# Kernel tuning notes

Measured on AMD Instinct MI355X. Metric: run time of the kernel, lower is better.

The kernel has to match this reference:

```python
import jax, jax.numpy as jnp
import numpy as np

N, E, C, NS, NB, NH = 20000, 320000, 64, 4, 8, 64
AVG_NEIGH = 16.0

def setup_inputs() -> dict:
    key = jax.random.key(0)
    ks = jax.random.split(key, 16)
    inp = {}
    inp['vectors'] = 0.35 * jax.random.normal(ks[0], (E, 3), jnp.float32)
    inp['node_scalars'] = jax.random.normal(ks[1], (N, C), jnp.float32)
    inp['node_vectors'] = jax.random.normal(ks[2], (N, C, 3), jnp.float32)
    inp['node_specie'] = jax.random.randint(ks[3], (N,), 0, NS)
    inp['senders'] = jax.random.randint(ks[4], (E,), 0, N)
    inp['receivers'] = jax.random.randint(ks[5], (E,), 0, N)
    # indexed skip linear: node irreps (64x0e+64x1o) -> 64x0e+64x1o+64x0e (scalars incl. gates)
    inp['W_skip_s'] = jax.random.normal(ks[6], (NS, C, 2 * C), jnp.float32) / np.sqrt(C)
    inp['W_skip_v'] = jax.random.normal(ks[7], (NS, C, C), jnp.float32) / np.sqrt(C)
    inp['W_up_s'] = jax.random.normal(ks[8], (C, C), jnp.float32) / np.sqrt(C)
    inp['W_up_v'] = jax.random.normal(ks[9], (C, C), jnp.float32) / np.sqrt(C)
    inp['W_mlp0'] = jax.random.normal(ks[10], (NB, NH), jnp.float32) / np.sqrt(NB)
    inp['W_mlp1'] = jax.random.normal(ks[11], (NH, NH), jnp.float32) / np.sqrt(NH)
    inp['W_mlp2'] = jax.random.normal(ks[12], (NH, 4 * C), jnp.float32) / np.sqrt(NH)
    inp['W_down_s'] = jax.random.normal(ks[13], (2 * C, 2 * C), jnp.float32) / np.sqrt(2 * C)
    inp['W_down_v'] = jax.random.normal(ks[14], (2 * C, C), jnp.float32) / np.sqrt(2 * C)
    return inp


def _forward(vectors, node_scalars, node_vectors, node_specie, senders, receivers,
             W_skip_s, W_skip_v, W_up_s, W_up_v, W_mlp0, W_mlp1, W_mlp2, W_down_s, W_down_v):
    n = node_scalars.shape[0]
    # --- self connection (specie-indexed linear) ---
    skip_s = jnp.einsum('ni,nio->no', node_scalars, W_skip_s[node_specie])   # [N,128]
    skip_v = jnp.einsum('nim,nio->nom', node_vectors, W_skip_v[node_specie]) # [N,64,3]
    # --- linear up ---
    s = node_scalars @ W_up_s                                  # [N,64]
    v = jnp.einsum('nim,io->nom', node_vectors, W_up_v)        # [N,64,3]
    ms, mv = s[senders], v[senders]                            # gather -> [E,64], [E,64,3]
    # --- spherical harmonics l=1, component normalization (|Y|=sqrt(3)) ---
    lengths = jnp.linalg.norm(vectors, axis=1, keepdims=True)  # [E,1]
    vhat = vectors / jnp.where(lengths == 0.0, 1.0, lengths)
    Y = jnp.sqrt(3.0) * vhat                                   # [E,3]
    # --- tensor product, filter_ir_out = {0e,1o} ---
    t1 = ms[:, :, None] * Y[:, None, :]                        # 0e x 1o -> 1o [E,64,3]
    t0 = jnp.einsum('ecm,em->ec', mv, Y) / jnp.sqrt(3.0)       # 1o x 1o -> 0e [E,64]
    msg_s = jnp.concatenate([ms, t0], axis=1)                  # [E,128]
    msg_v = jnp.concatenate([mv, t1], axis=1)                  # [E,128,3]
    # --- radial basis * polynomial envelope -> MLP ---
    x = lengths[:, 0]
    nvec = jnp.arange(1, NB + 1, dtype=vectors.dtype)
    safe_x = jnp.where(x == 0.0, 1.0, x)
    bess = jnp.sqrt(2.0) * jnp.sin(nvec * jnp.pi * x[:, None]) / safe_x[:, None]  # [E,8]
    u = jnp.clip(x, 0.0, 1.0)
    env = jnp.where(x < 1.0, 1.0 - 28.0 * u**6 + 48.0 * u**7 - 21.0 * u**8, 0.0)  # poly_envelope(5,2)
    h = jax.nn.swish((bess * env[:, None]) @ W_mlp0)
    h = jax.nn.swish(h @ W_mlp1)
    mix = h @ W_mlp2                                           # [E,256] = 128x0e + 128x1o weights
    mix = jnp.where(lengths == 0.0, 0.0, mix)
    msg_s = msg_s * mix[:, : 2 * C]
    msg_v = msg_v * mix[:, 2 * C :, None]
    # --- scatter-add to receivers, normalize by sqrt(avg_num_neighbors) ---
    inv = 1.0 / jnp.sqrt(AVG_NEIGH)
    agg_s = jnp.zeros((n, 2 * C), msg_s.dtype).at[receivers].add(msg_s) * inv
    agg_v = jnp.zeros((n, 2 * C, 3), msg_v.dtype).at[receivers].add(msg_v) * inv
    # --- linear down to 64x0e + 64x1o + 64x0e(gates) ---
    out_s = agg_s @ W_down_s + skip_s                          # [N,128]
    out_v = jnp.einsum('nim,io->nom', agg_v, W_down_v) + skip_v  # [N,64,3]
    # --- gate: swish on scalars, swish(gates) modulates vectors ---
    scal = jax.nn.swish(out_s[:, :C])
    gates = jax.nn.swish(out_s[:, C:])
    vec = out_v * gates[:, :, None]
    return jnp.concatenate([scal, vec.reshape(n, 3 * C)], axis=1)  # [N,256]


def reference(vectors, node_scalars, node_vectors, node_specie, senders, receivers,
              W_skip_s, W_skip_v, W_up_s, W_up_v, W_mlp0, W_mlp1, W_mlp2, W_down_s, W_down_v):
    return _forward(vectors, node_scalars, node_vectors, node_specie, senders, receivers,
                    W_skip_s, W_skip_v, W_up_s, W_up_v, W_mlp0, W_mlp1, W_mlp2, W_down_s, W_down_v)
```

## Files before the change

kernel.cpp:

```cpp
#include <hip/hip_runtime.h>
#include <math.h>

#define PI_F        3.14159265358979323846f
#define SQRT2_F     1.41421356237309515f
#define SQRT3_F     1.73205080756887729f
#define INV_SQRT3_F 0.57735026918962576f
#define INV_AVG     0.25f

#define N_NODES 20000
#define N_EDGES 320000

typedef float v2f __attribute__((ext_vector_type(2)));
typedef float v4f __attribute__((ext_vector_type(4)));

__device__ __forceinline__ float swish_f(float x) {
    return x / (1.f + __expf(-x));
}

__global__ __launch_bounds__(256, 8) void k_zero_cnt(int* __restrict__ cnt) {
    const int i = blockIdx.x * 256 + threadIdx.x;
    if (i < N_NODES) cnt[i] = 0;
}
__global__ __launch_bounds__(256, 8) void k_hist(const int* __restrict__ rcv,
                                                 int* __restrict__ cnt) {
    const int e = blockIdx.x * 256 + threadIdx.x;
    if (e < N_EDGES) atomicAdd(&cnt[rcv[e]], 1);
}
__global__ __launch_bounds__(1024) void k_scan(const int* __restrict__ cnt,
                                               int* __restrict__ cursor) {
    __shared__ int part[1024];
    const int t = threadIdx.x;
    const int base = t * 20;
    int s = 0;
    #pragma unroll
    for (int j = 0; j < 20; ++j) {
        const int idx = base + j;
        if (idx < N_NODES) s += cnt[idx];
    }
    part[t] = s;
    __syncthreads();
    for (int d = 1; d < 1024; d <<= 1) {
        const int v = (t >= d) ? part[t - d] : 0;
        __syncthreads();
        part[t] += v;
        __syncthreads();
    }
    int run = (t == 0) ? 0 : part[t - 1];
    for (int j = 0; j < 20; ++j) {
        const int idx = base + j;
        if (idx < N_NODES) { cursor[idx] = run; run += cnt[idx]; }
    }
}
__global__ __launch_bounds__(256, 8) void k_scatter(const int* __restrict__ rcv,
                                                    int* __restrict__ cursor,
                                                    int* __restrict__ perm) {
    const int e = blockIdx.x * 256 + threadIdx.x;
    if (e < N_EDGES) {
        const int pos = atomicAdd(&cursor[rcv[e]], 1);
        perm[pos] = e;
    }
}

__global__ __launch_bounds__(256) void k_node_up(
    const float* __restrict__ ns, const float* __restrict__ nv,
    const float* __restrict__ Wus, const float* __restrict__ Wuv,
    float* __restrict__ s_up, float* __restrict__ v_up,
    float* __restrict__ agg_s, float* __restrict__ agg_v)
{
    __shared__ v4f actu[16*64];

    const int tid  = threadIdx.x;
    const int lane = tid & 63;
    const int wq   = __builtin_amdgcn_readfirstlane(tid >> 6);
    const int nb   = blockIdx.x * 16;

    #pragma unroll
    for (int k = 0; k < 4; ++k) {
        const int idx = k*256 + tid;
        const int n = idx >> 6, i = idx & 63;
        const float* nvp = nv + (nb + n)*192 + 3*i;
        actu[idx] = (v4f){ns[(nb + n)*64 + i], nvp[0], nvp[1], nvp[2]};
    }
    __syncthreads();

    float acc[4] = {0.f, 0.f, 0.f, 0.f};
    float a0[4] = {}, a1[4] = {}, a2[4] = {};
    const v4f* aw = actu + wq*4*64;
    for (int i = 0; i < 64; ++i) {
        const float wu = Wus[i*64 + lane];
        const float wv = Wuv[i*64 + lane];
        #pragma unroll
        for (int j = 0; j < 4; ++j) {
            const v4f a = aw[j*64 + i];
            acc[j] = fmaf(a.x, wu, acc[j]);
            a0[j]  = fmaf(a.y, wv, a0[j]);
            a1[j]  = fmaf(a.z, wv, a1[j]);
            a2[j]  = fmaf(a.w, wv, a2[j]);
        }
    }
    const int cc = lane & 15, nt = lane >> 4;
    #pragma unroll
    for (int j = 0; j < 4; ++j) {
        const int n = nb + wq*4 + j;
        s_up[n*64 + cc*4 + nt] = acc[j];
        float* vq = v_up + n*192 + cc*12 + nt*3;
        vq[0] = a0[j]; vq[1] = a1[j]; vq[2] = a2[j];
        agg_s[n*128 + lane]      = 0.f;
        agg_s[n*128 + 64 + lane] = 0.f;
        #pragma unroll
        for (int k = 0; k < 6; ++k) agg_v[n*384 + k*64 + lane] = 0.f;
    }
}

__global__ __launch_bounds__(256, 4) void k_edge(
    const float* __restrict__ vecs,
    const int*   __restrict__ snd_idx, const int* __restrict__ rcv_idx,
    const int*   __restrict__ perm,
    const float* __restrict__ W0, const float* __restrict__ W1,
    const float* __restrict__ W2,
    const float* __restrict__ s_up, const float* __restrict__ v_up,
    float* __restrict__ agg_s, float* __restrict__ agg_v)
{
    __shared__ float hv[64*68];

    const int tid  = threadIdx.x;
    const int lane = tid & 63;
    const int wq   = __builtin_amdgcn_readfirstlane(tid >> 6);
    const int e0   = blockIdx.x * 64;
    const int c    = lane & 15, q = lane >> 4;

    const int pe_l  = perm[e0 + lane];
    const int rcv_l = rcv_idx[pe_l];
    const int snd_l = snd_idx[pe_l];
    const float vx_l = vecs[pe_l*3+0], vy_l = vecs[pe_l*3+1], vz_l = vecs[pe_l*3+2];
    const float x_l  = sqrtf(vx_l*vx_l + vy_l*vy_l + vz_l*vz_l);
    const float sx_l = (x_l == 0.f) ? 1.f : x_l;
    const float ys_l = SQRT3_F / sx_l;
    const float Y0_l = vx_l * ys_l, Y1_l = vy_l * ys_l, Y2_l = vz_l * ys_l;

    float s1_l, c1_l;
    __sincosf(PI_F * x_l, &s1_l, &c1_l);
    float pref_l;
    {
        const float u  = fminf(x_l, 1.f);
        const float u2 = u*u, u3 = u2*u;
        const float u6 = u3*u3, u7 = u6*u, u8 = u6*u2;
        const float env = (x_l < 1.f) ? (1.f - 28.f*u6 + 48.f*u7 - 21.f*u8) : 0.f;
        pref_l = (x_l == 0.f) ? 0.f : (SQRT2_F * env / sx_l);
    }

    float h1o[16];
    #pragma unroll 4
    for (int t = 0; t < 16; ++t) {
        const int le = wq*16 + t;
        const float sn0  = __shfl(s1_l, le);
        const float twoc = 2.f * __shfl(c1_l, le);
        const float pref = __shfl(pref_l, le);
        float acc1 = 0.f;
        float sn = sn0, snm1 = 0.f;
        #pragma unroll
        for (int b = 0; b < 8; ++b) {
            acc1 = fmaf(sn, W0[b*64 + lane], acc1);
            const float snext = fmaf(twoc, sn, -snm1);
            snm1 = sn; sn = snext;
        }
        h1o[t] = swish_f(pref * acc1);
    }
    {
        float* dst = hv + lane*68 + wq*16;
        #pragma unroll
        for (int k = 0; k < 4; ++k)
            ((v4f*)dst)[k] = (v4f){h1o[4*k], h1o[4*k+1], h1o[4*k+2], h1o[4*k+3]};
    }

    {
        v2f acc2[8];
        #pragma unroll
        for (int tp = 0; tp < 8; ++tp) acc2[tp] = (v2f){0.f, 0.f};
        const float* hbase = hv + wq*16;
        for (int i = 0; i < 64; ++i) {
            const float w = W1[i*64 + lane];
            const v2f wv = {w, w};
            const v4f* hp4 = (const v4f*)(hbase + i*68);
            #pragma unroll
            for (int k = 0; k < 4; ++k) {
                const v4f h4 = hp4[k];
                const v2f hlo = __builtin_shufflevector(h4, h4, 0, 1);
                const v2f hhi = __builtin_shufflevector(h4, h4, 2, 3);
                acc2[2*k]   = __builtin_elementwise_fma(hlo, wv, acc2[2*k]);
                acc2[2*k+1] = __builtin_elementwise_fma(hhi, wv, acc2[2*k+1]);
            }
        }
        float* dst = hv + lane*68 + wq*16;
        #pragma unroll
        for (int k = 0; k < 4; ++k)
            ((v4f*)dst)[k] = (v4f){swish_f(acc2[2*k][0]),   swish_f(acc2[2*k][1]),
                                   swish_f(acc2[2*k+1][0]), swish_f(acc2[2*k+1][1])};
    }
    __syncthreads();

    v2f mixp[8][4];
    #pragma unroll
    for (int tp = 0; tp < 8; ++tp)
        #pragma unroll
        for (int j = 0; j < 4; ++j) mixp[tp][j] = (v2f){0.f, 0.f};
    {
        const float* W2c = W2 + 64*wq + c;
        const float* hq  = hv + q*16;
        for (int i = 0; i < 64; ++i) {
            const float w0 = W2c[i*256 +  0];
            const float w1 = W2c[i*256 + 16];
            const float w2 = W2c[i*256 + 32];
            const float w3 = W2c[i*256 + 48];
            const v2f w0v = {w0,w0}, w1v = {w1,w1}, w2v = {w2,w2}, w3v = {w3,w3};
            const v4f* hp4 = (const v4f*)(hq + i*68);
            #pragma unroll
            for (int k = 0; k < 4; ++k) {
                const v4f h4 = hp4[k];
                const v2f hlo = __builtin_shufflevector(h4, h4, 0, 1);
                const v2f hhi = __builtin_shufflevector(h4, h4, 2, 3);
                mixp[2*k][0]   = __builtin_elementwise_fma(hlo, w0v, mixp[2*k][0]);
                mixp[2*k][1]   = __builtin_elementwise_fma(hlo, w1v, mixp[2*k][1]);
                mixp[2*k][2]   = __builtin_elementwise_fma(hlo, w2v, mixp[2*k][2]);
                mixp[2*k][3]   = __builtin_elementwise_fma(hlo, w3v, mixp[2*k][3]);
                mixp[2*k+1][0] = __builtin_elementwise_fma(hhi, w0v, mixp[2*k+1][0]);
                mixp[2*k+1][1] = __builtin_elementwise_fma(hhi, w1v, mixp[2*k+1][1]);
                mixp[2*k+1][2] = __builtin_elementwise_fma(hhi, w2v, mixp[2*k+1][2]);
                mixp[2*k+1][3] = __builtin_elementwise_fma(hhi, w3v, mixp[2*k+1][3]);
            }
        }
    }
    #define MIXR(t,j) (mixp[(t)>>1][j][(t)&1])

    int cur = -1;
    if (wq == 0) {
        float ra0=0.f, ra1=0.f, ra2=0.f, ra3=0.f;
        #pragma unroll
        for (int t = 0; t < 16; ++t) {
            const int sl  = (lane & 48) + t;
            const int rcv = __shfl(rcv_l, sl);
            const int snd = __shfl(snd_l, sl);
            if (rcv != cur) {
                if (cur >= 0) {
                    float* p = agg_s + cur*128 + c;
                    unsafeAtomicAdd(p,      ra0);
                    unsafeAtomicAdd(p + 16, ra1);
                    unsafeAtomicAdd(p + 32, ra2);
                    unsafeAtomicAdd(p + 48, ra3);
                }
                ra0 = ra1 = ra2 = ra3 = 0.f; cur = rcv;
            }
            const v4f sv = *(const v4f*)(s_up + snd*64 + c*4);
            ra0 = fmaf(sv.x, MIXR(t,0), ra0);
            ra1 = fmaf(sv.y, MIXR(t,1), ra1);
            ra2 = fmaf(sv.z, MIXR(t,2), ra2);
            ra3 = fmaf(sv.w, MIXR(t,3), ra3);
        }
        float* p = agg_s + cur*128 + c;
        unsafeAtomicAdd(p,      ra0);
        unsafeAtomicAdd(p + 16, ra1);
        unsafeAtomicAdd(p + 32, ra2);
        unsafeAtomicAdd(p + 48, ra3);
    } else if (wq == 1) {
        float ra0=0.f, ra1=0.f, ra2=0.f, ra3=0.f;
        #pragma unroll
        for (int t = 0; t < 16; ++t) {
            const int sl  = (lane & 48) + t;
            const int rcv = __shfl(rcv_l, sl);
            const int snd = __shfl(snd_l, sl);
            const float Y0 = __shfl(Y0_l, sl), Y1 = __shfl(Y1_l, sl), Y2 = __shfl(Y2_l, sl);
            if (rcv != cur) {
                if (cur >= 0) {
                    float* p = agg_s + cur*128 + 64 + c;
                    unsafeAtomicAdd(p,      ra0);
                    unsafeAtomicAdd(p + 16, ra1);
                    unsafeAtomicAdd(p + 32, ra2);
                    unsafeAtomicAdd(p + 48, ra3);
                }
                ra0 = ra1 = ra2 = ra3 = 0.f; cur = rcv;
            }
            const float* vb = v_up + snd*192 + c*12;
            const v4f f0 = *(const v4f*)(vb);
            const v4f f1 = *(const v4f*)(vb + 4);
            const v4f f2 = *(const v4f*)(vb + 8);
            const float t00 = (f0.x*Y0 + f0.y*Y1 + f0.z*Y2) * INV_SQRT3_F;
            const float t01 = (f0.w*Y0 + f1.x*Y1 + f1.y*Y2) * INV_SQRT3_F;
            const float t02 = (f1.z*Y0 + f1.w*Y1 + f2.x*Y2) * INV_SQRT3_F;
            const float t03 = (f2.y*Y0 + f2.z*Y1 + f2.w*Y2) * INV_SQRT3_F;
            ra0 = fmaf(t00, MIXR(t,0), ra0);
            ra1 = fmaf(t01, MIXR(t,1), ra1);
            ra2 = fmaf(t02, MIXR(t,2), ra2);
            ra3 = fmaf(t03, MIXR(t,3), ra3);
        }
        float* p = agg_s + cur*128 + 64 + c;
        unsafeAtomicAdd(p,      ra0);
        unsafeAtomicAdd(p + 16, ra1);
        unsafeAtomicAdd(p + 32, ra2);
        unsafeAtomicAdd(p + 48, ra3);
    } else if (wq == 2) {
        float rv[4][3];
        #pragma unroll
        for (int i = 0; i < 4; ++i) { rv[i][0]=0.f; rv[i][1]=0.f; rv[i][2]=0.f; }
        #pragma unroll
        for (int t = 0; t < 16; ++t) {
            const int sl  = (lane & 48) + t;
            const int rcv = __shfl(rcv_l, sl);
            const int snd = __shfl(snd_l, sl);
            if (rcv != cur) {
                if (cur >= 0) {
                    float* p = agg_v + cur*384 + c*3;
                    #pragma unroll
                    for (int ntl = 0; ntl < 4; ++ntl)
                        #pragma unroll
                        for (int m = 0; m < 3; ++m)
                            unsafeAtomicAdd(p + ntl*48 + m, rv[ntl][m]);
                }
                #pragma unroll
                for (int i = 0; i < 4; ++i) { rv[i][0]=0.f; rv[i][1]=0.f; rv[i][2]=0.f; }
                cur = rcv;
            }
            const float* vb = v_up + snd*192 + c*12;
            const v4f f0 = *(const v4f*)(vb);
            const v4f f1 = *(const v4f*)(vb + 4);
            const v4f f2 = *(const v4f*)(vb + 8);
            const float mx0 = MIXR(t,0);
            const float mx1 = MIXR(t,1);
            const float mx2 = MIXR(t,2);
            const float mx3 = MIXR(t,3);
            rv[0][0] = fmaf(f0.x, mx0, rv[0][0]);
            rv[0][1] = fmaf(f0.y, mx0, rv[0][1]);
            rv[0][2] = fmaf(f0.z, mx0, rv[0][2]);
            rv[1][0] = fmaf(f0.w, mx1, rv[1][0]);
            rv[1][1] = fmaf(f1.x, mx1, rv[1][1]);
            rv[1][2] = fmaf(f1.y, mx1, rv[1][2]);
            rv[2][0] = fmaf(f1.z, mx2, rv[2][0]);
            rv[2][1] = fmaf(f1.w, mx2, rv[2][1]);
            rv[2][2] = fmaf(f2.x, mx2, rv[2][2]);
            rv[3][0] = fmaf(f2.y, mx3, rv[3][0]);
            rv[3][1] = fmaf(f2.z, mx3, rv[3][1]);
            rv[3][2] = fmaf(f2.w, mx3, rv[3][2]);
        }
        float* p = agg_v + cur*384 + c*3;
        #pragma unroll
        for (int ntl = 0; ntl < 4; ++ntl)
            #pragma unroll
            for (int m = 0; m < 3; ++m)
                unsafeAtomicAdd(p + ntl*48 + m, rv[ntl][m]);
    } else {
        float rv[4][3];
        #pragma unroll
        for (int i = 0; i < 4; ++i) { rv[i][0]=0.f; rv[i][1]=0.f; rv[i][2]=0.f; }
        #pragma unroll
        for (int t = 0; t < 16; ++t) {
            const int sl  = (lane & 48) + t;
            const int rcv = __shfl(rcv_l, sl);
            const int snd = __shfl(snd_l, sl);
            const float Y0 = __shfl(Y0_l, sl), Y1 = __shfl(Y1_l, sl), Y2 = __shfl(Y2_l, sl);
            if (rcv != cur) {
                if (cur >= 0) {
                    float* p = agg_v + cur*384 + 192 + c*3;
                    #pragma unroll
                    for (int ntl = 0; ntl < 4; ++ntl)
                        #pragma unroll
                        for (int m = 0; m < 3; ++m)
                            unsafeAtomicAdd(p + ntl*48 + m, rv[ntl][m]);
                }
                #pragma unroll
                for (int i = 0; i < 4; ++i) { rv[i][0]=0.f; rv[i][1]=0.f; rv[i][2]=0.f; }
                cur = rcv;
            }
            const v4f sv = *(const v4f*)(s_up + snd*64 + c*4);
            const float mm0 = sv.x * MIXR(t,0);
            const float mm1 = sv.y * MIXR(t,1);
            const float mm2 = sv.z * MIXR(t,2);
            const float mm3 = sv.w * MIXR(t,3);
            rv[0][0] = fmaf(mm0, Y0, rv[0][0]);
            rv[0][1] = fmaf(mm0, Y1, rv[0][1]);
            rv[0][2] = fmaf(mm0, Y2, rv[0][2]);
            rv[1][0] = fmaf(mm1, Y0, rv[1][0]);
            rv[1][1] = fmaf(mm1, Y1, rv[1][1]);
            rv[1][2] = fmaf(mm1, Y2, rv[1][2]);
            rv[2][0] = fmaf(mm2, Y0, rv[2][0]);
            rv[2][1] = fmaf(mm2, Y1, rv[2][1]);
            rv[2][2] = fmaf(mm2, Y2, rv[2][2]);
            rv[3][0] = fmaf(mm3, Y0, rv[3][0]);
            rv[3][1] = fmaf(mm3, Y1, rv[3][1]);
            rv[3][2] = fmaf(mm3, Y2, rv[3][2]);
        }
        float* p = agg_v + cur*384 + 192 + c*3;
        #pragma unroll
        for (int ntl = 0; ntl < 4; ++ntl)
            #pragma unroll
            for (int m = 0; m < 3; ++m)
                unsafeAtomicAdd(p + ntl*48 + m, rv[ntl][m]);
    }
    #undef MIXR
}

__global__ __launch_bounds__(256) void k_node_down(
    const float* __restrict__ ns, const float* __restrict__ nv,
    const int*   __restrict__ spec_idx,
    const float* __restrict__ Wds, const float* __restrict__ Wdv,
    const float* __restrict__ Wsks, const float* __restrict__ Wskv,
    const float* __restrict__ agg_s, const float* __restrict__ agg_v,
    float* __restrict__ out)
{
    __shared__ v4f act[16*128];
    __shared__ v4f skp[16*64];
    __shared__ int bord[16];

    const int tid  = threadIdx.x;
    const int lane = tid & 63;
    const int wq   = __builtin_amdgcn_readfirstlane(tid >> 6);
    const int nb   = blockIdx.x * 16;

    if (tid < 16) {
        const int sp = spec_idx[nb + tid];
        int rank = 0;
        for (int j = 0; j < 16; ++j) {
            const int spj = spec_idx[nb + j];
            if (spj < sp || (spj == sp && j < tid)) ++rank;
        }
        bord[rank] = tid;
    }

    #pragma unroll
    for (int k = 0; k < 8; ++k) {
        const int idx = k*256 + tid;
        const int n = idx >> 7, i = idx & 127;
        const float a = agg_s[(nb + n)*128 + i] * INV_AVG;
        const float* av = agg_v + (nb + n)*384 + 3*i;
        act[idx] = (v4f){a, av[0]*INV_AVG, av[1]*INV_AVG, av[2]*INV_AVG};
    }
    #pragma unroll
    for (int k = 0; k < 4; ++k) {
        const int idx = k*256 + tid;
        const int n = idx >> 6, i = idx & 63;
        const float* nvp = nv + (nb + n)*192 + 3*i;
        skp[idx] = (v4f){ns[(nb + n)*64 + i], nvp[0], nvp[1], nvp[2]};
    }
    __syncthreads();

    int ln[4];
    #pragma unroll
    for (int j = 0; j < 4; ++j)
        ln[j] = bord[wq*4 + j];

    float s0[4] = {}, s1[4] = {}, v0[4] = {}, v1[4] = {}, v2[4] = {};

    for (int i = 0; i < 128; ++i) {
        const float wd0 = Wds[i*128 + lane];
        const float wd1 = Wds[i*128 + 64 + lane];
        const float wdv = Wdv[i*64 + lane];
        #pragma unroll
        for (int j = 0; j < 4; ++j) {
            const v4f a = act[ln[j]*128 + i];
            s0[j] = fmaf(a.x, wd0, s0[j]);
            s1[j] = fmaf(a.x, wd1, s1[j]);
            v0[j] = fmaf(a.y, wdv, v0[j]);
            v1[j] = fmaf(a.z, wdv, v1[j]);
            v2[j] = fmaf(a.w, wdv, v2[j]);
        }
    }

    const float* Ws_j[4]; const float* Wv_j[4];
    #pragma unroll
    for (int j = 0; j < 4; ++j) {
        const int spec = __builtin_amdgcn_readfirstlane(spec_idx[nb + ln[j]]);
        Ws_j[j] = Wsks + spec*8192;
        Wv_j[j] = Wskv + spec*4096;
    }
    for (int i = 0; i < 64; ++i) {
        #pragma unroll
        for (int j = 0; j < 4; ++j) {
            const v4f a = skp[ln[j]*64 + i];
            s0[j] = fmaf(a.x, Ws_j[j][i*128 + lane], s0[j]);
            s1[j] = fmaf(a.x, Ws_j[j][i*128 + 64 + lane], s1[j]);
            const float wv = Wv_j[j][i*64 + lane];
            v0[j] = fmaf(a.y, wv, v0[j]);
            v1[j] = fmaf(a.z, wv, v1[j]);
            v2[j] = fmaf(a.w, wv, v2[j]);
        }
    }

    #pragma unroll
    for (int j = 0; j < 4; ++j) {
        const int n = nb + ln[j];
        const float scal = swish_f(s0[j]);
        const float gate = swish_f(s1[j]);
        out[n*256 + lane]            = scal;
        out[n*256 + 64 + lane*3 + 0] = v0[j] * gate;
        out[n*256 + 64 + lane*3 + 1] = v1[j] * gate;
        out[n*256 + 64 + lane*3 + 2] = v2[j] * gate;
    }
}

extern "C" void kernel_launch(void* const* d_in, const int* in_sizes, int n_in,
                              void* d_out, int out_size, void* d_ws, size_t ws_size,
                              hipStream_t stream)
{
    (void)in_sizes; (void)n_in; (void)out_size; (void)ws_size;

    const float* vectors      = (const float*)d_in[0];
    const float* node_scalars = (const float*)d_in[1];
    const float* node_vectors = (const float*)d_in[2];
    const int*   node_specie  = (const int*)d_in[3];
    const int*   senders      = (const int*)d_in[4];
    const int*   receivers    = (const int*)d_in[5];
    const float* W_skip_s     = (const float*)d_in[6];
    const float* W_skip_v     = (const float*)d_in[7];
    const float* W_up_s       = (const float*)d_in[8];
    const float* W_up_v       = (const float*)d_in[9];
    const float* W_mlp0       = (const float*)d_in[10];
    const float* W_mlp1       = (const float*)d_in[11];
    const float* W_mlp2       = (const float*)d_in[12];
    const float* W_down_s     = (const float*)d_in[13];
    const float* W_down_v     = (const float*)d_in[14];
    float* out = (float*)d_out;

    float* ws    = (float*)d_ws;
    float* s_up  = ws;
    float* v_up  = s_up + 1280000;
    float* agg_s = v_up + 3840000;
    float* agg_v = agg_s + 2560000;
    int*   perm  = (int*)(agg_v + 7680000);
    int*   cnt    = (int*)agg_s;
    int*   cursor = cnt + 20000;

    hipLaunchKernelGGL(k_zero_cnt, dim3(79),   dim3(256),  0, stream, cnt);
    hipLaunchKernelGGL(k_hist,     dim3(1250), dim3(256),  0, stream, receivers, cnt);
    hipLaunchKernelGGL(k_scan,     dim3(1),    dim3(1024), 0, stream, cnt, cursor);
    hipLaunchKernelGGL(k_scatter,  dim3(1250), dim3(256),  0, stream, receivers, cursor, perm);

    hipLaunchKernelGGL(k_node_up, dim3(1250), dim3(256), 0, stream,
        node_scalars, node_vectors, W_up_s, W_up_v, s_up, v_up, agg_s, agg_v);
    hipLaunchKernelGGL(k_edge, dim3(5000), dim3(256), 0, stream,
        vectors, senders, receivers, perm, W_mlp0, W_mlp1, W_mlp2,
        s_up, v_up, agg_s, agg_v);
    hipLaunchKernelGGL(k_node_down, dim3(1250), dim3(256), 0, stream,
        node_scalars, node_vectors, node_specie, W_down_s, W_down_v,
        W_skip_s, W_skip_v, agg_s, agg_v, out);
}
```

Baseline: 485.8 us.

## Cut k_edge register pressure via LDS edge metadata and half-split mix accumulation

Per-edge metadata (receiver, sender, Y, sin/cos, prefactor) is written to shared memory instead of being held in registers and broadcast with shuffles. The W2 mix matmul and scatter now run in two halves of 8 edges, which halves the mix accumulator array. Launch bounds rise from 4 to 6 waves so register use must fit a higher occupancy target. This reloads W2 twice and may emit extra atomics at the half boundary. Separately, k_node_down drops its per-block species sort and processes nodes in natural order, which removes that setup work but may make the skip-weight loads less uniform within a wave.

```diff
diff --git a/kernel.cpp b/kernel.cpp
--- a/kernel.cpp
+++ b/kernel.cpp
@@ -112,7 +112,7 @@
     }
 }
 
-__global__ __launch_bounds__(256, 4) void k_edge(
+__global__ __launch_bounds__(256, 6) void k_edge(
     const float* __restrict__ vecs,
     const int*   __restrict__ snd_idx, const int* __restrict__ rcv_idx,
     const int*   __restrict__ perm,
@@ -122,42 +122,44 @@
     float* __restrict__ agg_s, float* __restrict__ agg_v)
 {
     __shared__ float hv[64*68];
+    __shared__ v4f   meta[64*2];
 
     const int tid  = threadIdx.x;
     const int lane = tid & 63;
     const int wq   = __builtin_amdgcn_readfirstlane(tid >> 6);
     const int e0   = blockIdx.x * 64;
     const int c    = lane & 15, q = lane >> 4;
-
-    const int pe_l  = perm[e0 + lane];
-    const int rcv_l = rcv_idx[pe_l];
-    const int snd_l = snd_idx[pe_l];
-    const float vx_l = vecs[pe_l*3+0], vy_l = vecs[pe_l*3+1], vz_l = vecs[pe_l*3+2];
-    const float x_l  = sqrtf(vx_l*vx_l + vy_l*vy_l + vz_l*vz_l);
-    const float sx_l = (x_l == 0.f) ? 1.f : x_l;
-    const float ys_l = SQRT3_F / sx_l;
-    const float Y0_l = vx_l * ys_l, Y1_l = vy_l * ys_l, Y2_l = vz_l * ys_l;
-
-    float s1_l, c1_l;
-    __sincosf(PI_F * x_l, &s1_l, &c1_l);
-    float pref_l;
+    const float* mb = (const float*)meta;
+
     {
-        const float u  = fminf(x_l, 1.f);
+        const int pe  = perm[e0 + lane];
+        const int rcv = rcv_idx[pe];
+        const int snd = snd_idx[pe];
+        const float vx = vecs[pe*3+0], vy = vecs[pe*3+1], vz = vecs[pe*3+2];
+        const float x  = sqrtf(vx*vx + vy*vy + vz*vz);
+        const float sx = (x == 0.f) ? 1.f : x;
+        const float ys = SQRT3_F / sx;
+        float s1, c1;
+        __sincosf(PI_F * x, &s1, &c1);
+        const float u  = fminf(x, 1.f);
         const float u2 = u*u, u3 = u2*u;
         const float u6 = u3*u3, u7 = u6*u, u8 = u6*u2;
-        const float env = (x_l < 1.f) ? (1.f - 28.f*u6 + 48.f*u7 - 21.f*u8) : 0.f;
-        pref_l = (x_l == 0.f) ? 0.f : (SQRT2_F * env / sx_l);
+        const float env = (x < 1.f) ? (1.f - 28.f*u6 + 48.f*u7 - 21.f*u8) : 0.f;
+        const float pref = (x == 0.f) ? 0.f : (SQRT2_F * env / sx);
+        meta[lane*2 + 0] = (v4f){__int_as_float(rcv), __int_as_float(snd),
+                                 vx*ys, vy*ys};
+        meta[lane*2 + 1] = (v4f){vz*ys, s1, c1, pref};
     }
 
     float h1o[16];
     #pragma unroll 4
     for (int t = 0; t < 16; ++t) {
         const int le = wq*16 + t;
-        const float sn0  = __shfl(s1_l, le);
-        const float twoc = 2.f * __shfl(c1_l, le);
-        const float pref = __shfl(pref_l, le);
+        const v4f m1 = meta[le*2 + 1];
+        const float pref = m1.w;
+        const float twoc = 2.f * m1.z;
         float acc1 = 0.f;
-        float sn = sn0, snm1 = 0.f;
+        float sn = m1.y, snm1 = 0.f;
         #pragma unroll
         for (int b = 0; b < 8; ++b) {
             acc1 = fmaf(sn, W0[b*64 + lane], acc1);
@@ -199,202 +201,211 @@
     }
     __syncthreads();
 
-    v2f mixp[8][4];
-    #pragma unroll
-    for (int tp = 0; tp < 8; ++tp)
-        #pragma unroll
-        for (int j = 0; j < 4; ++j) mixp[tp][j] = (v2f){0.f, 0.f};
-    {
-        const float* W2c = W2 + 64*wq + c;
-        const float* hq  = hv + q*16;
-        for (int i = 0; i < 64; ++i) {
-            const float w0 = W2c[i*256 +  0];
-            const float w1 = W2c[i*256 + 16];
-            const float w2 = W2c[i*256 + 32];
-            const float w3 = W2c[i*256 + 48];
-            const v2f w0v = {w0,w0}, w1v = {w1,w1}, w2v = {w2,w2}, w3v = {w3,w3};
-            const v4f* hp4 = (const v4f*)(hq + i*68);
-            #pragma unroll
-            for (int k = 0; k < 4; ++k) {
-                const v4f h4 = hp4[k];
-                const v2f hlo = __builtin_shufflevector(h4, h4, 0, 1);
-                const v2f hhi = __builtin_shufflevector(h4, h4, 2, 3);
-                mixp[2*k][0]   = __builtin_elementwise_fma(hlo, w0v, mixp[2*k][0]);
-                mixp[2*k][1]   = __builtin_elementwise_fma(hlo, w1v, mixp[2*k][1]);
-                mixp[2*k][2]   = __builtin_elementwise_fma(hlo, w2v, mixp[2*k][2]);
-                mixp[2*k][3]   = __builtin_elementwise_fma(hlo, w3v, mixp[2*k][3]);
-                mixp[2*k+1][0] = __builtin_elementwise_fma(hhi, w0v, mixp[2*k+1][0]);
-                mixp[2*k+1][1] = __builtin_elementwise_fma(hhi, w1v, mixp[2*k+1][1]);
-                mixp[2*k+1][2] = __builtin_elementwise_fma(hhi, w2v, mixp[2*k+1][2]);
-                mixp[2*k+1][3] = __builtin_elementwise_fma(hhi, w3v, mixp[2*k+1][3]);
+    #pragma unroll
+    for (int hf = 0; hf < 2; ++hf) {
+        v2f mixp[4][4];
+        #pragma unroll
+        for (int tp = 0; tp < 4; ++tp)
+            #pragma unroll
+            for (int j = 0; j < 4; ++j) mixp[tp][j] = (v2f){0.f, 0.f};
+        {
+            const float* W2c = W2 + 64*wq + c;
+            const float* hq  = hv + q*16 + hf*8;
+            for (int i = 0; i < 64; ++i) {
+                const float w0 = W2c[i*256 +  0];
+                const float w1 = W2c[i*256 + 16];
+                const float w2 = W2c[i*256 + 32];
+                const float w3 = W2c[i*256 + 48];
+                const v2f w0v = {w0,w0}, w1v = {w1,w1}, w2v = {w2,w2}, w3v = {w3,w3};
+                const v4f* hp4 = (const v4f*)(hq + i*68);
+                #pragma unroll
+                for (int k = 0; k < 2; ++k) {
+                    const v4f h4 = hp4[k];
+                    const v2f hlo = __builtin_shufflevector(h4, h4, 0, 1);
+                    const v2f hhi = __builtin_shufflevector(h4, h4, 2, 3);
+                    mixp[2*k][0]   = __builtin_elementwise_fma(hlo, w0v, mixp[2*k][0]);
+                    mixp[2*k][1]   = __builtin_elementwise_fma(hlo, w1v, mixp[2*k][1]);
+                    mixp[2*k][2]   = __builtin_elementwise_fma(hlo, w2v, mixp[2*k][2]);
+                    mixp[2*k][3]   = __builtin_elementwise_fma(hlo, w3v, mixp[2*k][3]);
+                    mixp[2*k+1][0] = __builtin_elementwise_fma(hhi, w0v, mixp[2*k+1][0]);
+                    mixp[2*k+1][1] = __builtin_elementwise_fma(hhi, w1v, mixp[2*k+1][1]);
+                    mixp[2*k+1][2] = __builtin_elementwise_fma(hhi, w2v, mixp[2*k+1][2]);
+                    mixp[2*k+1][3] = __builtin_elementwise_fma(hhi, w3v, mixp[2*k+1][3]);
+                }
             }
         }
-    }
-    #define MIXR(t,j) (mixp[(t)>>1][j][(t)&1])
-
-    int cur = -1;
-    if (wq == 0) {
-        float ra0=0.f, ra1=0.f, ra2=0.f, ra3=0.f;
-        #pragma unroll
-        for (int t = 0; t < 16; ++t) {
-            const int sl  = (lane & 48) + t;
-            const int rcv = __shfl(rcv_l, sl);
-            const int snd = __shfl(snd_l, sl);
-            if (rcv != cur) {
-                if (cur >= 0) {
-                    float* p = agg_s + cur*128 + c;
-                    unsafeAtomicAdd(p,      ra0);
-                    unsafeAtomicAdd(p + 16, ra1);
-                    unsafeAtomicAdd(p + 32, ra2);
-                    unsafeAtomicAdd(p + 48, ra3);
+        #define MIXR(t,j) (mixp[(t)>>1][j][(t)&1])
+
+        int cur = -1;
+        if (wq == 0) {
+            float ra0=0.f, ra1=0.f, ra2=0.f, ra3=0.f;
+            #pragma unroll
+            for (int t = 0; t < 8; ++t) {
+                const int el = (lane & 48) + hf*8 + t;
+                const v2f rs = *(const v2f*)(mb + el*8);
+                const int rcv = __float_as_int(rs.x);
+                const int snd = __float_as_int(rs.y);
+                if (rcv != cur) {
+                    if (cur >= 0) {
+                        float* p = agg_s + cur*128 + c;
+                        unsafeAtomicAdd(p,      ra0);
+                        unsafeAtomicAdd(p + 16, ra1);
+                        unsafeAtomicAdd(p + 32, ra2);
+                        unsafeAtomicAdd(p + 48, ra3);
+                    }
+                    ra0 = ra1 = ra2 = ra3 = 0.f; cur = rcv;
                 }
-                ra0 = ra1 = ra2 = ra3 = 0.f; cur = rcv;
+                const v4f sv = *(const v4f*)(s_up + snd*64 + c*4);
+                ra0 = fmaf(sv.x, MIXR(t,0), ra0);
+                ra1 = fmaf(sv.y, MIXR(t,1), ra1);
+                ra2 = fmaf(sv.z, MIXR(t,2), ra2);
+                ra3 = fmaf(sv.w, MIXR(t,3), ra3);
             }
-            const v4f sv = *(const v4f*)(s_up + snd*64 + c*4);
-            ra0 = fmaf(sv.x, MIXR(t,0), ra0);
-            ra1 = fmaf(sv.y, MIXR(t,1), ra1);
-            ra2 = fmaf(sv.z, MIXR(t,2), ra2);
-            ra3 = fmaf(sv.w, MIXR(t,3), ra3);
-        }
-        float* p = agg_s + cur*128 + c;
-        unsafeAtomicAdd(p,      ra0);
-        unsafeAtomicAdd(p + 16, ra1);
-        unsafeAtomicAdd(p + 32, ra2);
-        unsafeAtomicAdd(p + 48, ra3);
-    } else if (wq == 1) {
-        float ra0=0.f, ra1=0.f, ra2=0.f, ra3=0.f;
-        #pragma unroll
-        for (int t = 0; t < 16; ++t) {
-            const int sl  = (lane & 48) + t;
-            const int rcv = __shfl(rcv_l, sl);
-            const int snd = __shfl(snd_l, sl);
-            const float Y0 = __shfl(Y0_l, sl), Y1 = __shfl(Y1_l, sl), Y2 = __shfl(Y2_l, sl);
-            if (rcv != cur) {
-                if (cur >= 0) {
-                    float* p = agg_s + cur*128 + 64 + c;
-                    unsafeAtomicAdd(p,      ra0);
-                    unsafeAtomicAdd(p + 16, ra1);
-                    unsafeAtomicAdd(p + 32, ra2);
-                    unsafeAtomicAdd(p + 48, ra3);
+            float* p = agg_s + cur*128 + c;
+            unsafeAtomicAdd(p,      ra0);
+            unsafeAtomicAdd(p + 16, ra1);
+            unsafeAtomicAdd(p + 32, ra2);
+            unsafeAtomicAdd(p + 48, ra3);
+        } else if (wq == 1) {
+            float ra0=0.f, ra1=0.f, ra2=0.f, ra3=0.f;
+            #pragma unroll
+            for (int t = 0; t < 8; ++t) {
+                const int el = (lane & 48) + hf*8 + t;
+                const v4f m0 = meta[el*2];
+                const float Y2 = mb[el*8 + 4];
+                const int rcv = __float_as_int(m0.x);
+                const int snd = __float_as_int(m0.y);
+                const float Y0 = m0.z, Y1 = m0.w;
+                if (rcv != cur) {
+                    if (cur >= 0) {
+                        float* p = agg_s + cur*128 + 64 + c;
+                        unsafeAtomicAdd(p,      ra0);
+                        unsafeAtomicAdd(p + 16, ra1);
+                        unsafeAtomicAdd(p + 32, ra2);
+                        unsafeAtomicAdd(p + 48, ra3);
+                    }
+                    ra0 = ra1 = ra2 = ra3 = 0.f; cur = rcv;
                 }
-                ra0 = ra1 = ra2 = ra3 = 0.f; cur = rcv;
+                const float* vb = v_up + snd*192 + c*12;
+                const v4f f0 = *(const v4f*)(vb);
+                const v4f f1 = *(const v4f*)(vb + 4);
+                const v4f f2 = *(const v4f*)(vb + 8);
+                const float t00 = (f0.x*Y0 + f0.y*Y1 + f0.z*Y2) * INV_SQRT3_F;
+                const float t01 = (f0.w*Y0 + f1.x*Y1 + f1.y*Y2) * INV_SQRT3_F;
+                const float t02 = (f1.z*Y0 + f1.w*Y1 + f2.x*Y2) * INV_SQRT3_F;
+                const float t03 = (f2.y*Y0 + f2.z*Y1 + f2.w*Y2) * INV_SQRT3_F;
+                ra0 = fmaf(t00, MIXR(t,0), ra0);
+                ra1 = fmaf(t01, MIXR(t,1), ra1);
+                ra2 = fmaf(t02, MIXR(t,2), ra2);
+                ra3 = fmaf(t03, MIXR(t,3), ra3);
             }
-            const float* vb = v_up + snd*192 + c*12;
-            const v4f f0 = *(const v4f*)(vb);
-            const v4f f1 = *(const v4f*)(vb + 4);
-            const v4f f2 = *(const v4f*)(vb + 8);
-            const float t00 = (f0.x*Y0 + f0.y*Y1 + f0.z*Y2) * INV_SQRT3_F;
-            const float t01 = (f0.w*Y0 + f1.x*Y1 + f1.y*Y2) * INV_SQRT3_F;
-            const float t02 = (f1.z*Y0 + f1.w*Y1 + f2.x*Y2) * INV_SQRT3_F;
-            const float t03 = (f2.y*Y0 + f2.z*Y1 + f2.w*Y2) * INV_SQRT3_F;
-            ra0 = fmaf(t00, MIXR(t,0), ra0);
-            ra1 = fmaf(t01, MIXR(t,1), ra1);
-            ra2 = fmaf(t02, MIXR(t,2), ra2);
-            ra3 = fmaf(t03, MIXR(t,3), ra3);
-        }
-        float* p = agg_s + cur*128 + 64 + c;
-        unsafeAtomicAdd(p,      ra0);
-        unsafeAtomicAdd(p + 16, ra1);
-        unsafeAtomicAdd(p + 32, ra2);
-        unsafeAtomicAdd(p + 48, ra3);
-    } else if (wq == 2) {
-        float rv[4][3];
-        #pragma unroll
-        for (int i = 0; i < 4; ++i) { rv[i][0]=0.f; rv[i][1]=0.f; rv[i][2]=0.f; }
-        #pragma unroll
-        for (int t = 0; t < 16; ++t) {
-            const int sl  = (lane & 48) + t;
-            const int rcv = __shfl(rcv_l, sl);
-            const int snd = __shfl(snd_l, sl);
-            if (rcv != cur) {
-                if (cur >= 0) {
-                    float* p = agg_v + cur*384 + c*3;
+            float* p = agg_s + cur*128 + 64 + c;
+            unsafeAtomicAdd(p,      ra0);
+            unsafeAtomicAdd(p + 16, ra1);
+            unsafeAtomicAdd(p + 32, ra2);
+            unsafeAtomicAdd(p + 48, ra3);
+        } else if (wq == 2) {
+            float rv[4][3];
+            #pragma unroll
+            for (int i = 0; i < 4; ++i) { rv[i][0]=0.f; rv[i][1]=0.f; rv[i][2]=0.f; }
+            #pragma unroll
+            for (int t = 0; t < 8; ++t) {
+                const int el = (lane & 48) + hf*8 + t;
+                const v2f rs = *(const v2f*)(mb + el*8);
+                const int rcv = __float_as_int(rs.x);
+                const int snd = __float_as_int(rs.y);
+                if (rcv != cur) {
+                    if (cur >= 0) {
+                        float* p = agg_v + cur*384 + c*3;
+                        #pragma unroll
+                        for (int ntl = 0; ntl < 4; ++ntl)
+                            #pragma unroll
+                            for (int m = 0; m < 3; ++m)
+                                unsafeAtomicAdd(p + ntl*48 + m, rv[ntl][m]);
+                    }
                     #pragma unroll
-                    for (int ntl = 0; ntl < 4; ++ntl)
+                    for (int i = 0; i < 4; ++i) { rv[i][0]=0.f; rv[i][1]=0.f; rv[i][2]=0.f; }
+                    cur = rcv;
+                }
+                const float* vb = v_up + snd*192 + c*12;
+                const v4f f0 = *(const v4f*)(vb);
+                const v4f f1 = *(const v4f*)(vb + 4);
+                const v4f f2 = *(const v4f*)(vb + 8);
+                const float mx0 = MIXR(t,0);
+                const float mx1 = MIXR(t,1);
+                const float mx2 = MIXR(t,2);
+                const float mx3 = MIXR(t,3);
+                rv[0][0] = fmaf(f0.x, mx0, rv[0][0]);
+                rv[0][1] = fmaf(f0.y, mx0, rv[0][1]);
+                rv[0][2] = fmaf(f0.z, mx0, rv[0][2]);
+                rv[1][0] = fmaf(f0.w, mx1, rv[1][0]);
+                rv[1][1] = fmaf(f1.x, mx1, rv[1][1]);
+                rv[1][2] = fmaf(f1.y, mx1, rv[1][2]);
+                rv[2][0] = fmaf(f1.z, mx2, rv[2][0]);
+                rv[2][1] = fmaf(f1.w, mx2, rv[2][1]);
+                rv[2][2] = fmaf(f2.x, mx2, rv[2][2]);
+                rv[3][0] = fmaf(f2.y, mx3, rv[3][0]);
+                rv[3][1] = fmaf(f2.z, mx3, rv[3][1]);
+                rv[3][2] = fmaf(f2.w, mx3, rv[3][2]);
+            }
+            float* p = agg_v + cur*384 + c*3;
+            #pragma unroll
+            for (int ntl = 0; ntl < 4; ++ntl)
+                #pragma unroll
+                for (int m = 0; m < 3; ++m)
+                    unsafeAtomicAdd(p + ntl*48 + m, rv[ntl][m]);
+        } else {
+            float rv[4][3];
+            #pragma unroll
+            for (int i = 0; i < 4; ++i) { rv[i][0]=0.f; rv[i][1]=0.f; rv[i][2]=0.f; }
+            #pragma unroll
+            for (int t = 0; t < 8; ++t) {
+                const int el = (lane & 48) + hf*8 + t;
+                const v4f m0 = meta[el*2];
+                const float Y2 = mb[el*8 + 4];
+                const int rcv = __float_as_int(m0.x);
+                const int snd = __float_as_int(m0.y);
+                const float Y0 = m0.z, Y1 = m0.w;
+                if (rcv != cur) {
+                    if (cur >= 0) {
+                        float* p = agg_v + cur*384 + 192 + c*3;
                         #pragma unroll
-                        for (int m = 0; m < 3; ++m)
-                            unsafeAtomicAdd(p + ntl*48 + m, rv[ntl][m]);
+                        for (int ntl = 0; ntl < 4; ++ntl)
+                            #pragma unroll
+                            for (int m = 0; m < 3; ++m)
+                                unsafeAtomicAdd(p + ntl*48 + m, rv[ntl][m]);
+                    }
+                    #pragma unroll
+                    for (int i = 0; i < 4; ++i) { rv[i][0]=0.f; rv[i][1]=0.f; rv[i][2]=0.f; }
+                    cur = rcv;
                 }
+                const v4f sv = *(const v4f*)(s_up + snd*64 + c*4);
+                const float mm0 = sv.x * MIXR(t,0);
+                const float mm1 = sv.y * MIXR(t,1);
+                const float mm2 = sv.z * MIXR(t,2);
+                const float mm3 = sv.w * MIXR(t,3);
+                rv[0][0] = fmaf(mm0, Y0, rv[0][0]);
+                rv[0][1] = fmaf(mm0, Y1, rv[0][1]);
+                rv[0][2] = fmaf(mm0, Y2, rv[0][2]);
+                rv[1][0] = fmaf(mm1, Y0, rv[1][0]);
+                rv[1][1] = fmaf(mm1, Y1, rv[1][1]);
+                rv[1][2] = fmaf(mm1, Y2, rv[1][2]);
+                rv[2][0] = fmaf(mm2, Y0, rv[2][0]);
+                rv[2][1] = fmaf(mm2, Y1, rv[2][1]);
+                rv[2][2] = fmaf(mm2, Y2, rv[2][2]);
+                rv[3][0] = fmaf(mm3, Y0, rv[3][0]);
+                rv[3][1] = fmaf(mm3, Y1, rv[3][1]);
+                rv[3][2] = fmaf(mm3, Y2, rv[3][2]);
+            }
+            float* p = agg_v + cur*384 + 192 + c*3;
+            #pragma unroll
+            for (int ntl = 0; ntl < 4; ++ntl)
                 #pragma unroll
-                for (int i = 0; i < 4; ++i) { rv[i][0]=0.f; rv[i][1]=0.f; rv[i][2]=0.f; }
-                cur = rcv;
-            }
-            const float* vb = v_up + snd*192 + c*12;
-            const v4f f0 = *(const v4f*)(vb);
-            const v4f f1 = *(const v4f*)(vb + 4);
-            const v4f f2 = *(const v4f*)(vb + 8);
-            const float mx0 = MIXR(t,0);
-            const float mx1 = MIXR(t,1);
-            const float mx2 = MIXR(t,2);
-            const float mx3 = MIXR(t,3);
-            rv[0][0] = fmaf(f0.x, mx0, rv[0][0]);
-            rv[0][1] = fmaf(f0.y, mx0, rv[0][1]);
-            rv[0][2] = fmaf(f0.z, mx0, rv[0][2]);
-            rv[1][0] = fmaf(f0.w, mx1, rv[1][0]);
-            rv[1][1] = fmaf(f1.x, mx1, rv[1][1]);
-            rv[1][2] = fmaf(f1.y, mx1, rv[1][2]);
-            rv[2][0] = fmaf(f1.z, mx2, rv[2][0]);
-            rv[2][1] = fmaf(f1.w, mx2, rv[2][1]);
-            rv[2][2] = fmaf(f2.x, mx2, rv[2][2]);
-            rv[3][0] = fmaf(f2.y, mx3, rv[3][0]);
-            rv[3][1] = fmaf(f2.z, mx3, rv[3][1]);
-            rv[3][2] = fmaf(f2.w, mx3, rv[3][2]);
-        }
-        float* p = agg_v + cur*384 + c*3;
-        #pragma unroll
-        for (int ntl = 0; ntl < 4; ++ntl)
-            #pragma unroll
-            for (int m = 0; m < 3; ++m)
-                unsafeAtomicAdd(p + ntl*48 + m, rv[ntl][m]);
-    } else {
-        float rv[4][3];
-        #pragma unroll
-        for (int i = 0; i < 4; ++i) { rv[i][0]=0.f; rv[i][1]=0.f; rv[i][2]=0.f; }
-        #pragma unroll
-        for (int t = 0; t < 16; ++t) {
-            const int sl  = (lane & 48) + t;
-            const int rcv = __shfl(rcv_l, sl);
-            const int snd = __shfl(snd_l, sl);
-            const float Y0 = __shfl(Y0_l, sl), Y1 = __shfl(Y1_l, sl), Y2 = __shfl(Y2_l, sl);
-            if (rcv != cur) {
-                if (cur >= 0) {
-                    float* p = agg_v + cur*384 + 192 + c*3;
-                    #pragma unroll
-                    for (int ntl = 0; ntl < 4; ++ntl)
-                        #pragma unroll
-                        for (int m = 0; m < 3; ++m)
-                            unsafeAtomicAdd(p + ntl*48 + m, rv[ntl][m]);
-                }
-                #pragma unroll
-                for (int i = 0; i < 4; ++i) { rv[i][0]=0.f; rv[i][1]=0.f; rv[i][2]=0.f; }
-                cur = rcv;
-            }
-            const v4f sv = *(const v4f*)(s_up + snd*64 + c*4);
-            const float mm0 = sv.x * MIXR(t,0);
-            const float mm1 = sv.y * MIXR(t,1);
-            const float mm2 = sv.z * MIXR(t,2);
-            const float mm3 = sv.w * MIXR(t,3);
-            rv[0][0] = fmaf(mm0, Y0, rv[0][0]);
-            rv[0][1] = fmaf(mm0, Y1, rv[0][1]);
-            rv[0][2] = fmaf(mm0, Y2, rv[0][2]);
-            rv[1][0] = fmaf(mm1, Y0, rv[1][0]);
-            rv[1][1] = fmaf(mm1, Y1, rv[1][1]);
-            rv[1][2] = fmaf(mm1, Y2, rv[1][2]);
-            rv[2][0] = fmaf(mm2, Y0, rv[2][0]);
-            rv[2][1] = fmaf(mm2, Y1, rv[2][1]);
-            rv[2][2] = fmaf(mm2, Y2, rv[2][2]);
-            rv[3][0] = fmaf(mm3, Y0, rv[3][0]);
-            rv[3][1] = fmaf(mm3, Y1, rv[3][1]);
-            rv[3][2] = fmaf(mm3, Y2, rv[3][2]);
-        }
-        float* p = agg_v + cur*384 + 192 + c*3;
-        #pragma unroll
-        for (int ntl = 0; ntl < 4; ++ntl)
-            #pragma unroll
-            for (int m = 0; m < 3; ++m)
-                unsafeAtomicAdd(p + ntl*48 + m, rv[ntl][m]);
-    }
-    #undef MIXR
+                for (int m = 0; m < 3; ++m)
+                    unsafeAtomicAdd(p + ntl*48 + m, rv[ntl][m]);
+        }
+        #undef MIXR
+    }
 }
 
 __global__ __launch_bounds__(256) void k_node_down(
@@ -407,22 +418,11 @@
 {
     __shared__ v4f act[16*128];
     __shared__ v4f skp[16*64];
-    __shared__ int bord[16];
 
     const int tid  = threadIdx.x;
     const int lane = tid & 63;
     const int wq   = __builtin_amdgcn_readfirstlane(tid >> 6);
     const int nb   = blockIdx.x * 16;
-
-    if (tid < 16) {
-        const int sp = spec_idx[nb + tid];
-        int rank = 0;
-        for (int j = 0; j < 16; ++j) {
-            const int spj = spec_idx[nb + j];
-            if (spj < sp || (spj == sp && j < tid)) ++rank;
-        }
-        bord[rank] = tid;
-    }
 
     #pragma unroll
     for (int k = 0; k < 8; ++k) {
@@ -441,20 +441,16 @@
     }
     __syncthreads();
 
-    int ln[4];
-    #pragma unroll
-    for (int j = 0; j < 4; ++j)
-        ln[j] = bord[wq*4 + j];
-
     float s0[4] = {}, s1[4] = {}, v0[4] = {}, v1[4] = {}, v2[4] = {};
 
+    const v4f* aw = act + wq*4*128;
     for (int i = 0; i < 128; ++i) {
         const float wd0 = Wds[i*128 + lane];
         const float wd1 = Wds[i*128 + 64 + lane];
         const float wdv = Wdv[i*64 + lane];
         #pragma unroll
         for (int j = 0; j < 4; ++j) {
-            const v4f a = act[ln[j]*128 + i];
+            const v4f a = aw[j*128 + i];
             s0[j] = fmaf(a.x, wd0, s0[j]);
             s1[j] = fmaf(a.x, wd1, s1[j]);
             v0[j] = fmaf(a.y, wdv, v0[j]);
@@ -463,17 +459,19 @@
         }
     }
 
+    const int n0 = nb + wq*4;
     const float* Ws_j[4]; const float* Wv_j[4];
     #pragma unroll
     for (int j = 0; j < 4; ++j) {
-        const int spec = __builtin_amdgcn_readfirstlane(spec_idx[nb + ln[j]]);
+        const int spec = __builtin_amdgcn_readfirstlane(spec_idx[n0 + j]);
         Ws_j[j] = Wsks + spec*8192;
         Wv_j[j] = Wskv + spec*4096;
     }
+    const v4f* sw = skp + wq*4*64;
     for (int i = 0; i < 64; ++i) {
         #pragma unroll
         for (int j = 0; j < 4; ++j) {
-            const v4f a = skp[ln[j]*64 + i];
+            const v4f a = sw[j*64 + i];
             s0[j] = fmaf(a.x, Ws_j[j][i*128 + lane], s0[j]);
             s1[j] = fmaf(a.x, Ws_j[j][i*128 + 64 + lane], s1[j]);
             const float wv = Wv_j[j][i*64 + lane];
@@ -485,7 +483,7 @@
 
     #pragma unroll
     for (int j = 0; j < 4; ++j) {
-        const int n = nb + ln[j];
+        const int n = n0 + j;
         const float scal = swish_f(s0[j]);
         const float gate = swish_f(s1[j]);
         out[n*256 + lane]            = scal;
```

After: 615.2 us. 1.27x slower.
